# Kernel optimization log

Hardware: AMD Instinct MI355X
Metric: run time of the kernel (lower is better)

Reference implementation:

```python
import jax, jax.numpy as jnp
import numpy as np

B = 8192            # batch size
L_AVG = 50          # average bag length
TOTAL = B * L_AVG   # total indices per feature (fixed for jit)
NUM_EMB = 1_000_000
DIM = 64
NUM_TABLES = 4


def _make_offsets(key, total, batch):
    # jagged bag boundaries: offsets[0]=0, offsets[-1]=total, interior sorted
    cuts = jnp.sort(jax.random.randint(key, (batch - 1,), 0, total + 1, dtype=jnp.int32))
    return jnp.concatenate([jnp.zeros((1,), jnp.int32), cuts,
                            jnp.full((1,), total, jnp.int32)])


def setup_inputs() -> dict:
    key = jax.random.key(0)
    ks = jax.random.split(key, 3 * NUM_TABLES)
    inp = {}
    for t in range(NUM_TABLES):
        inp[f"W{t}"] = jax.random.normal(ks[3 * t], (NUM_EMB, DIM), dtype=jnp.float32) * 0.02
        inp[f"values{t}"] = jax.random.randint(ks[3 * t + 1], (TOTAL,), 0, NUM_EMB, dtype=jnp.int32)
        inp[f"offsets{t}"] = _make_offsets(ks[3 * t + 2], TOTAL, B)
    return inp


def _pool_mean(W, values, offsets):
    # EmbeddingBag(mode='mean', include_last_offset=True):
    # bag i = mean of W[values[offsets[i]:offsets[i+1]]]; empty bag -> zeros
    pos = jnp.arange(values.shape[0])
    seg = jnp.searchsorted(offsets, pos, side='right') - 1   # bag id per index
    emb = W[values]                                          # [TOTAL, DIM] gather
    summed = jax.ops.segment_sum(emb, seg, num_segments=B)   # [B, DIM]
    counts = (offsets[1:] - offsets[:-1]).astype(W.dtype)    # [B]
    return summed / jnp.maximum(counts, 1.0)[:, None]


def reference(W0, W1, W2, W3,
              values0, values1, values2, values3,
              offsets0, offsets1, offsets2, offsets3):
    pooled = [
        _pool_mean(W0, values0, offsets0),
        _pool_mean(W1, values1, offsets1),
        _pool_mean(W2, values2, offsets2),
        _pool_mean(W3, values3, offsets3),
    ]
    # KeyedTensor values: concat along embedding dim -> [B, sum(D_t)]
    return jnp.concatenate(pooled, axis=1)
```

## Files before the change

### kernel.cpp

```cpp
#include <hip/hip_runtime.h>


#define NBAGS 8192
#define DIM 64

__global__ __launch_bounds__(256) void ebc_kernel(
    const float* __restrict__ W0, const int* __restrict__ v0, const int* __restrict__ o0,
    const float* __restrict__ W1, const int* __restrict__ v1, const int* __restrict__ o1,
    const float* __restrict__ W2, const int* __restrict__ v2, const int* __restrict__ o2,
    const float* __restrict__ W3, const int* __restrict__ v3, const int* __restrict__ o3,
    float* __restrict__ out)
{
    const int table = threadIdx.x >> 6;
    const int lane  = threadIdx.x & 63;
    const int g     = lane >> 4;
    const int s     = lane & 15;
    const int bag   = blockIdx.x;

    const float* W; const int* vals; const int* offs;
    if      (table == 0) { W = W0; vals = v0; offs = o0; }
    else if (table == 1) { W = W1; vals = v1; offs = o1; }
    else if (table == 2) { W = W2; vals = v2; offs = o2; }
    else                 { W = W3; vals = v3; offs = o3; }

    const int start = offs[bag];
    const int end   = offs[bag + 1];

    float4 acc0 = {0,0,0,0}, acc1 = {0,0,0,0}, acc2 = {0,0,0,0}, acc3 = {0,0,0,0};

    for (int base = start; base < end; base += 64) {
        const int rem = end - base;
        const int n   = rem < 64 ? rem : 64;
        const int nm1 = n - 1;

        int v = 0;
        if (lane < n) v = vals[base + lane];

        float4 t[16];
        float  w[16];
        #pragma unroll
        for (int k = 0; k < 16; ++k) {
            const int r   = 4 * k + g;
            const int src = r < nm1 ? r : nm1;
            const int idx = __shfl(v, src);
            t[k] = *(const float4*)(W + (size_t)idx * DIM + s * 4);
            w[k] = (r < n) ? 1.0f : 0.0f;
        }
        #pragma unroll
        for (int k = 0; k < 16; ++k) {
            float4* a = (k & 3) == 0 ? &acc0 : (k & 3) == 1 ? &acc1
                       : (k & 3) == 2 ? &acc2 : &acc3;
            a->x = fmaf(t[k].x, w[k], a->x);
            a->y = fmaf(t[k].y, w[k], a->y);
            a->z = fmaf(t[k].z, w[k], a->z);
            a->w = fmaf(t[k].w, w[k], a->w);
        }
    }

    float4 acc;
    acc.x = (acc0.x + acc1.x) + (acc2.x + acc3.x);
    acc.y = (acc0.y + acc1.y) + (acc2.y + acc3.y);
    acc.z = (acc0.z + acc1.z) + (acc2.z + acc3.z);
    acc.w = (acc0.w + acc1.w) + (acc2.w + acc3.w);

    acc.x += __shfl_xor(acc.x, 16); acc.y += __shfl_xor(acc.y, 16);
    acc.z += __shfl_xor(acc.z, 16); acc.w += __shfl_xor(acc.w, 16);
    acc.x += __shfl_xor(acc.x, 32); acc.y += __shfl_xor(acc.y, 32);
    acc.z += __shfl_xor(acc.z, 32); acc.w += __shfl_xor(acc.w, 32);

    const int cnt = end - start;
    const float inv = cnt > 0 ? 1.0f / (float)cnt : 0.0f;

    if (g == 0) {
        float4 r;
        r.x = acc.x * inv; r.y = acc.y * inv; r.z = acc.z * inv; r.w = acc.w * inv;
        *(float4*)(out + (size_t)bag * (4 * DIM) + table * DIM + s * 4) = r;
    }
}

extern "C" void kernel_launch(void* const* d_in, const int* in_sizes, int n_in,
                              void* d_out, int out_size, void* d_ws, size_t ws_size,
                              hipStream_t stream) {
    const float* W0 = (const float*)d_in[0];
    const int*   v0 = (const int*)  d_in[1];
    const int*   o0 = (const int*)  d_in[2];
    const float* W1 = (const float*)d_in[3];
    const int*   v1 = (const int*)  d_in[4];
    const int*   o1 = (const int*)  d_in[5];
    const float* W2 = (const float*)d_in[6];
    const int*   v2 = (const int*)  d_in[7];
    const int*   o2 = (const int*)  d_in[8];
    const float* W3 = (const float*)d_in[9];
    const int*   v3 = (const int*)  d_in[10];
    const int*   o3 = (const int*)  d_in[11];
    float* out = (float*)d_out;

    ebc_kernel<<<NBAGS, 256, 0, stream>>>(W0, v0, o0, W1, v1, o1,
                                          W2, v2, o2, W3, v3, o3, out);
}
```

Measured before the change: 76.75 us.

## Process eight bags per block with software-pipelined index prefetch

Each block now handles eight consecutive bags per table instead of one. The offsets are loaded once into lane registers and read with shuffles, and the index chunk for the next bag or chunk is loaded while the current chunk's row gathers are still in flight. The aim is to hide the index-load latency and cut per-block launch and offset-load overhead. The cost is fewer blocks (1024 instead of 8192) and serial work per wave, which lowers parallelism and may hurt latency hiding for the random row gathers.

After: 85.24 us. +11.0%, slower.

```diff
diff --git a/kernel.cpp b/kernel.cpp
--- a/kernel.cpp
+++ b/kernel.cpp
@@ -3,6 +3,8 @@
 
 #define NBAGS 8192
 #define DIM 64
+#define NB 8
+#define OFF(i) __shfl(off_reg, (i))
 
 __global__ __launch_bounds__(256) void ebc_kernel(
     const float* __restrict__ W0, const int* __restrict__ v0, const int* __restrict__ o0,
@@ -15,7 +17,7 @@
     const int lane  = threadIdx.x & 63;
     const int g     = lane >> 4;
     const int s     = lane & 15;
-    const int bag   = blockIdx.x;
+    const int b0    = blockIdx.x * NB;
 
     const float* W; const int* vals; const int* offs;
     if      (table == 0) { W = W0; vals = v0; offs = o0; }
@@ -23,58 +25,73 @@
     else if (table == 2) { W = W2; vals = v2; offs = o2; }
     else                 { W = W3; vals = v3; offs = o3; }
 
-    const int start = offs[bag];
-    const int end   = offs[bag + 1];
+    int off_reg = 0;
+    if (lane <= NB) off_reg = offs[b0 + lane];
+
+    int cb    = 0;
+    int cbase = OFF(0);
+    int cend  = OFF(1);
+    int cn    = cend - cbase; cn = cn < 0 ? 0 : (cn > 64 ? 64 : cn);
+    int v_cur = 0;
+    if (lane < cn) v_cur = vals[cbase + lane];
 
     float4 acc0 = {0,0,0,0}, acc1 = {0,0,0,0}, acc2 = {0,0,0,0}, acc3 = {0,0,0,0};
 
-    for (int base = start; base < end; base += 64) {
-        const int rem = end - base;
-        const int n   = rem < 64 ? rem : 64;
-        const int nm1 = n - 1;
+    while (cb < NB) {
+        int nb = cb, nbase = cbase + 64;
+        if (nbase >= cend) { nb = cb + 1; nbase = (nb < NB) ? OFF(nb) : 0; }
 
-        int v = 0;
-        if (lane < n) v = vals[base + lane];
-
+        const int srcmax = cn > 0 ? cn - 1 : 0;
         float4 t[16];
-        float  w[16];
         #pragma unroll
         for (int k = 0; k < 16; ++k) {
             const int r   = 4 * k + g;
-            const int src = r < nm1 ? r : nm1;
-            const int idx = __shfl(v, src);
+            const int src = r < srcmax ? r : srcmax;
+            const int idx = __shfl(v_cur, src);
             t[k] = *(const float4*)(W + (size_t)idx * DIM + s * 4);
-            w[k] = (r < n) ? 1.0f : 0.0f;
         }
+
+        int nn = 0, nend = 0, v_nxt = 0;
+        if (nb < NB) {
+            nend = OFF(nb + 1);
+            nn   = nend - nbase; nn = nn < 0 ? 0 : (nn > 64 ? 64 : nn);
+            if (lane < nn) v_nxt = vals[nbase + lane];
+        }
+
         #pragma unroll
         for (int k = 0; k < 16; ++k) {
+            const float wk = (4 * k + g < cn) ? 1.0f : 0.0f;
             float4* a = (k & 3) == 0 ? &acc0 : (k & 3) == 1 ? &acc1
                        : (k & 3) == 2 ? &acc2 : &acc3;
-            a->x = fmaf(t[k].x, w[k], a->x);
-            a->y = fmaf(t[k].y, w[k], a->y);
-            a->z = fmaf(t[k].z, w[k], a->z);
-            a->w = fmaf(t[k].w, w[k], a->w);
+            a->x = fmaf(t[k].x, wk, a->x);
+            a->y = fmaf(t[k].y, wk, a->y);
+            a->z = fmaf(t[k].z, wk, a->z);
+            a->w = fmaf(t[k].w, wk, a->w);
         }
-    }
 
-    float4 acc;
-    acc.x = (acc0.x + acc1.x) + (acc2.x + acc3.x);
-    acc.y = (acc0.y + acc1.y) + (acc2.y + acc3.y);
-    acc.z = (acc0.z + acc1.z) + (acc2.z + acc3.z);
-    acc.w = (acc0.w + acc1.w) + (acc2.w + acc3.w);
+        if (nb != cb) {
+            float4 acc;
+            acc.x = (acc0.x + acc1.x) + (acc2.x + acc3.x);
+            acc.y = (acc0.y + acc1.y) + (acc2.y + acc3.y);
+            acc.z = (acc0.z + acc1.z) + (acc2.z + acc3.z);
+            acc.w = (acc0.w + acc1.w) + (acc2.w + acc3.w);
+            acc.x += __shfl_xor(acc.x, 16); acc.y += __shfl_xor(acc.y, 16);
+            acc.z += __shfl_xor(acc.z, 16); acc.w += __shfl_xor(acc.w, 16);
+            acc.x += __shfl_xor(acc.x, 32); acc.y += __shfl_xor(acc.y, 32);
+            acc.z += __shfl_xor(acc.z, 32); acc.w += __shfl_xor(acc.w, 32);
 
-    acc.x += __shfl_xor(acc.x, 16); acc.y += __shfl_xor(acc.y, 16);
-    acc.z += __shfl_xor(acc.z, 16); acc.w += __shfl_xor(acc.w, 16);
-    acc.x += __shfl_xor(acc.x, 32); acc.y += __shfl_xor(acc.y, 32);
-    acc.z += __shfl_xor(acc.z, 32); acc.w += __shfl_xor(acc.w, 32);
+            const int len = cend - OFF(cb);
+            const float inv = len > 0 ? 1.0f / (float)len : 0.0f;
+            if (g == 0) {
+                float4 r;
+                r.x = acc.x * inv; r.y = acc.y * inv;
+                r.z = acc.z * inv; r.w = acc.w * inv;
+                *(float4*)(out + (size_t)(b0 + cb) * (4 * DIM) + table * DIM + s * 4) = r;
+            }
+            acc0 = acc1 = acc2 = acc3 = make_float4(0.f, 0.f, 0.f, 0.f);
+        }
 
-    const int cnt = end - start;
-    const float inv = cnt > 0 ? 1.0f / (float)cnt : 0.0f;
-
-    if (g == 0) {
-        float4 r;
-        r.x = acc.x * inv; r.y = acc.y * inv; r.z = acc.z * inv; r.w = acc.w * inv;
-        *(float4*)(out + (size_t)bag * (4 * DIM) + table * DIM + s * 4) = r;
+        cb = nb; cbase = nbase; cend = nend; cn = nn; v_cur = v_nxt;
     }
 }
 
@@ -95,6 +112,6 @@
     const int*   o3 = (const int*)  d_in[11];
     float* out = (float*)d_out;
 
-    ebc_kernel<<<NBAGS, 256, 0, stream>>>(W0, v0, o0, W1, v1, o1,
-                                          W2, v2, o2, W3, v3, o3, out);
+    ebc_kernel<<<NBAGS / NB, 256, 0, stream>>>(W0, v0, o0, W1, v1, o1,
+                                               W2, v2, o2, W3, v3, o3, out);
 }
```
